# Performance work log

Measured on AMD Instinct MI355X. Metric: run time of the kernel, lower is better.

## Reference

```python
import jax, jax.numpy as jnp
from jax import lax
import numpy as np

B, L = 256, 4096
H, RL, RH = 128, 2, 32   # num_hiddens, residual layers, residual hiddens
K, D = 512, 64           # codebook size, embedding dim
CC = 0.25                # commitment cost


def conv1d(x, w, b=None, stride=1, pad=0, circular=False):
    # x: (N,C,L), w: (O,I,k)
    if circular and pad > 0:
        x = jnp.pad(x, ((0, 0), (0, 0), (pad, pad)), mode='wrap')
        pad = 0
    y = lax.conv_general_dilated(x, w, (stride,), [(pad, pad)],
                                 dimension_numbers=('NCH', 'OIH', 'NCH'))
    return y if b is None else y + b[None, :, None]


def convt1d(x, w, b):
    # PyTorch ConvTranspose1d(k=4, s=2, p=1); w: (I,O,4). out_len = 2*L.
    wt = jnp.flip(jnp.swapaxes(w, 0, 1), -1)  # (O,I,4)
    y = lax.conv_general_dilated(x, wt, (1,), [(2, 2)], lhs_dilation=(2,),
                                 dimension_numbers=('NCH', 'OIH', 'NCH'))
    return y + b[None, :, None]


def res_stack(x, w1s, w2s):
    for i in range(w1s.shape[0]):
        h = conv1d(jax.nn.relu(x), w1s[i], None, 1, 1, circular=True)
        h = conv1d(jax.nn.relu(h), w2s[i], None, 1, 0)
        x = x + h
    return jax.nn.relu(x)


def setup_inputs() -> dict:
    key = jax.random.key(0)
    ks = iter(jax.random.split(key, 64))

    def w(*shape):
        fan_in = int(np.prod(shape[1:]))
        return jax.random.normal(next(ks), shape, jnp.float32) / np.sqrt(fan_in)

    def bias(n):
        return jax.random.uniform(next(ks), (n,), jnp.float32, -0.05, 0.05)

    inp = {'x': jax.random.normal(next(ks), (B, 1, L), jnp.float32)}
    # Encoder
    inp['enc_c1_w'] = w(H // 2, 1, 4);      inp['enc_c1_b'] = bias(H // 2)
    inp['enc_c2_w'] = w(H, H // 2, 4);      inp['enc_c2_b'] = bias(H)
    inp['enc_c3_w'] = w(H, H, 4);           inp['enc_c3_b'] = bias(H)
    inp['enc_c4_w'] = w(H, H, 4);           inp['enc_c4_b'] = bias(H)
    inp['enc_cf_w'] = w(H, H, 3);           inp['enc_cf_b'] = bias(H)
    inp['enc_res_w1'] = w(RL, RH, H, 3)
    inp['enc_res_w2'] = w(RL, H, RH, 1)
    # pre-VQ 1x1 conv
    inp['prevq_w'] = w(D, H, 1);            inp['prevq_b'] = bias(D)
    # codebook: uniform(-1/K, 1/K) as in source
    inp['emb'] = jax.random.uniform(next(ks), (K, D), jnp.float32, -1.0 / K, 1.0 / K)
    # Decoder
    inp['dec_init_w'] = w(H, D, 3);         inp['dec_init_b'] = bias(H)
    inp['dec_res_w1'] = w(RL, RH, H, 3)
    inp['dec_res_w2'] = w(RL, H, RH, 1)
    inp['ct0_w'] = w(H, H, 4);              inp['ct0_b'] = bias(H)
    inp['ct1_w'] = w(H, H, 4);              inp['ct1_b'] = bias(H)
    inp['ct2_w'] = w(H, H // 2, 4);         inp['ct2_b'] = bias(H // 2)
    inp['ct3_w'] = w(H // 2, 1, 4);         inp['ct3_b'] = bias(1)
    return inp


def _forward(x, enc_c1_w, enc_c1_b, enc_c2_w, enc_c2_b, enc_c3_w, enc_c3_b,
             enc_c4_w, enc_c4_b, enc_cf_w, enc_cf_b, enc_res_w1, enc_res_w2,
             prevq_w, prevq_b, emb, dec_init_w, dec_init_b, dec_res_w1,
             dec_res_w2, ct0_w, ct0_b, ct1_w, ct1_b, ct2_w, ct2_b, ct3_w, ct3_b):
    sg = lax.stop_gradient
    relu = jax.nn.relu
    # ---- Encoder (circular padding) ----
    z = relu(conv1d(x, enc_c1_w, enc_c1_b, 2, 1, circular=True))
    z = relu(conv1d(z, enc_c2_w, enc_c2_b, 2, 1, circular=True))
    z = relu(conv1d(z, enc_c3_w, enc_c3_b, 2, 1, circular=True))
    z = relu(conv1d(z, enc_c4_w, enc_c4_b, 2, 1, circular=True))
    z = conv1d(z, enc_cf_w, enc_cf_b, 1, 1, circular=True)
    z = res_stack(z, enc_res_w1, enc_res_w2)
    z = conv1d(z, prevq_w, prevq_b, 1, 0)        # (B, D, T)
    # ---- Vector quantizer ----
    z_t = jnp.transpose(z, (0, 2, 1))            # (B, T, D)
    flat = z_t.reshape(-1, D)                    # (BT, D)
    dist = (jnp.sum(flat ** 2, axis=1, keepdims=True)
            + jnp.sum(emb ** 2, axis=1)
            - 2.0 * flat @ emb.T)                # (BT, K)
    idx = jnp.argmin(dist, axis=1)               # (BT,)
    enc = jax.nn.one_hot(idx, K, dtype=flat.dtype)
    q = (enc @ emb).reshape(z_t.shape)           # (B, T, D)
    e_loss = jnp.mean((sg(q) - z_t) ** 2)
    q_loss = jnp.mean((q - sg(z_t)) ** 2)
    loss = q_loss + CC * e_loss
    q_st = z_t + sg(q - z_t)                     # straight-through
    avg = jnp.mean(enc, axis=0)
    perplexity = jnp.exp(-jnp.sum(avg * jnp.log(avg + 1e-10)))
    quantized = jnp.transpose(q_st, (0, 2, 1))   # (B, D, T)
    # ---- Decoder ----
    h = conv1d(quantized, dec_init_w, dec_init_b, 1, 1)
    h = res_stack(h, dec_res_w1, dec_res_w2)
    h = relu(convt1d(h, ct0_w, ct0_b))
    h = relu(convt1d(h, ct1_w, ct1_b))
    h = relu(convt1d(h, ct2_w, ct2_b))
    x_recon = convt1d(h, ct3_w, ct3_b)           # (B, 1, L)
    return loss, x_recon, perplexity


def reference(x, enc_c1_w, enc_c1_b, enc_c2_w, enc_c2_b, enc_c3_w, enc_c3_b,
              enc_c4_w, enc_c4_b, enc_cf_w, enc_cf_b, enc_res_w1, enc_res_w2,
              prevq_w, prevq_b, emb, dec_init_w, dec_init_b, dec_res_w1,
              dec_res_w2, ct0_w, ct0_b, ct1_w, ct1_b, ct2_w, ct2_b, ct3_w, ct3_b):
    return _forward(x, enc_c1_w, enc_c1_b, enc_c2_w, enc_c2_b, enc_c3_w,
                    enc_c3_b, enc_c4_w, enc_c4_b, enc_cf_w, enc_cf_b,
                    enc_res_w1, enc_res_w2, prevq_w, prevq_b, emb,
                    dec_init_w, dec_init_b, dec_res_w1, dec_res_w2,
                    ct0_w, ct0_b, ct1_w, ct1_b, ct2_w, ct2_b, ct3_w, ct3_b)
```

## Files before the change

### kernel.cpp

```cpp
#include <hip/hip_runtime.h>

#define DEVI __device__ __forceinline__

typedef __bf16 bf16x8 __attribute__((ext_vector_type(8)));
typedef float f32x4 __attribute__((ext_vector_type(4)));

DEVI ushort f2b(float f) {
  uint b = __float_as_uint(f);
  uint r = (b + 0x7FFFu + ((b >> 16) & 1u)) >> 16;
  return (ushort)r;
}
DEVI float b2f(ushort u) { return __uint_as_float(((uint)u) << 16); }

struct PrepArgs {
  int nw;
  int tot[20];
  const float* src[20];
  ushort* dst[20];
  int ci[20], co[20], sco[20], sci[20], sk[20];
};

__global__ __launch_bounds__(256)
void prep_all(PrepArgs a, int total) {
  int i = blockIdx.x * 256 + threadIdx.x;
  if (i >= total) return;
  int w = 0;
  while (i >= a.tot[w]) { i -= a.tot[w]; ++w; }
  const int li = i;
  const int CI = a.ci[w];
  int ciX = i % CI;
  int rest = i / CI;
  int coX = rest % a.co[w];
  int k = rest / a.co[w];
  a.dst[w][li] = f2b(a.src[w][coX * a.sco[w] + ciX * a.sci[w] + k * a.sk[w]]);
}

__global__ __launch_bounds__(256)
void enc1_bf(const float* __restrict__ x, const float* __restrict__ w1,
             const float* __restrict__ b1, ushort* __restrict__ out) {
  __shared__ float xl[516];
  __shared__ float w1s[256];
  __shared__ float b1s[64];
  const int n = blockIdx.x >> 3;
  const int t0 = (blockIdx.x & 7) << 8;
  const int tid = threadIdx.x;
  const float* xb = x + ((size_t)n << 12);
  for (int j = tid; j < 514; j += 256)
    xl[j] = xb[(2 * t0 - 1 + j + 4096) & 4095];
  if (tid < 256) w1s[tid] = w1[tid];
  if (tid < 64) b1s[tid] = b1[tid];
  __syncthreads();

  const int oct = tid & 7;
  float4 w4[8];
  float bs[8];
  #pragma unroll
  for (int e = 0; e < 8; ++e) {
    w4[e] = *reinterpret_cast<const float4*>(&w1s[(oct * 8 + e) * 4]);
    bs[e] = b1s[oct * 8 + e];
  }
  ushort* ob = out + (((size_t)n * 2048 + t0) << 6) + tid * 8;
  #pragma unroll
  for (int it = 0; it < 8; ++it) {
    const int tl = it * 32 + (tid >> 3);
    const float x0 = xl[2 * tl], x1 = xl[2 * tl + 1], x2 = xl[2 * tl + 2], x3 = xl[2 * tl + 3];
    uint pack[4];
    #pragma unroll
    for (int h = 0; h < 4; ++h) {
      float s0 = fmaf(w4[2 * h].x, x0, fmaf(w4[2 * h].y, x1,
                 fmaf(w4[2 * h].z, x2, fmaf(w4[2 * h].w, x3, bs[2 * h]))));
      float s1 = fmaf(w4[2 * h + 1].x, x0, fmaf(w4[2 * h + 1].y, x1,
                 fmaf(w4[2 * h + 1].z, x2, fmaf(w4[2 * h + 1].w, x3, bs[2 * h + 1]))));
      pack[h] = (uint)f2b(fmaxf(s0, 0.0f)) | ((uint)f2b(fmaxf(s1, 0.0f)) << 16);
    }
    *reinterpret_cast<uint4*>(ob + it * 2048) = uint4{pack[0], pack[1], pack[2], pack[3]};
  }
}

template<int CI, int CO, int K, int S, bool CIRC, bool GATHER, int NT, int WAVES_CO,
         int NCHUNK = 1>
__global__ __launch_bounds__(256)
void conv_mfma(const ushort* __restrict__ in, const ushort* __restrict__ wb,
               const float* __restrict__ bias, const ushort* __restrict__ resid,
               ushort* __restrict__ out, const int* __restrict__ gidx,
               int Tin, int in_relu, int out_relu) {
  constexpr int PAD = (K > 1) ? 1 : 0;
  constexpr int TT = NT * 16;
  constexpr int SPAN = S * (TT - 1) + K;
  constexpr int CICH = CI / NCHUNK;
  constexpr int CIGc = CICH / 8;
  constexpr int COT = CO / 16;
  constexpr int WCOT = COT / WAVES_CO;
  constexpr int WAVES_T = 4 / WAVES_CO;
  constexpr int WTT = NT / WAVES_T;
  constexpr int KSH = (S == 2) ? 1 : 0;
  static_assert(CICH % 32 == 0 && COT % WAVES_CO == 0 && NT % WAVES_T == 0, "");

  __shared__ __align__(16) ushort xs[SPAN * CICH];

  const int Tout = Tin / S;
  const int tilesPerB = Tout / TT;
  const int n = blockIdx.x / tilesPerB;
  const int t0 = (blockIdx.x % tilesPerB) * TT;
  const int tid = threadIdx.x;
  const int wid = tid >> 6, lane = tid & 63;
  const int l15 = lane & 15, l4 = lane >> 4;

  const int t_in0 = S * t0 - PAD;
  const ushort* inb = GATHER ? in : in + (size_t)n * Tin * CI;

  const int wco = wid % WAVES_CO;
  const int wt = wid / WAVES_CO;
  const int co_base = wco * WCOT * 16;
  const int t_base = wt * WTT * 16;

  f32x4 acc[WTT][WCOT] = {};

  for (int h = 0; h < NCHUNK; ++h) {
    if (h) __syncthreads();
    for (int i = tid; i < SPAN * CIGc; i += 256) {
      int t = i / CIGc, g = i - (i / CIGc) * CIGc;
      int tg = t_in0 + t;
      uint4 v;
      if (CIRC) {
        tg = (tg < 0) ? tg + Tin : (tg >= Tin ? tg - Tin : tg);
        v = *reinterpret_cast<const uint4*>(inb + (size_t)tg * CI + h * CICH + g * 8);
      } else if (GATHER) {
        if ((unsigned)tg < (unsigned)Tin) {
          int id = gidx[n * Tin + tg];
          v = *reinterpret_cast<const uint4*>(inb + (size_t)id * CI + h * CICH + g * 8);
        } else
          v = uint4{0, 0, 0, 0};
      } else {
        if ((unsigned)tg < (unsigned)Tin)
          v = *reinterpret_cast<const uint4*>(inb + (size_t)tg * CI + h * CICH + g * 8);
        else
          v = uint4{0, 0, 0, 0};
      }
      if (in_relu) {
        ushort* pv = reinterpret_cast<ushort*>(&v);
        #pragma unroll
        for (int e = 0; e < 8; ++e) pv[e] = (pv[e] & 0x8000) ? 0 : pv[e];
      }
      *reinterpret_cast<uint4*>(&xs[t * CICH + ((g ^ ((t >> KSH) & (CIGc - 1))) * 8)]) = v;
    }
    __syncthreads();

    for (int cc = 0; cc < CICH / 32; ++cc) {
      const int ccg = h * (CICH / 32) + cc;
      bf16x8 bk[K][WCOT];
      #pragma unroll
      for (int k = 0; k < K; ++k)
        #pragma unroll
        for (int c = 0; c < WCOT; ++c)
          bk[k][c] = __builtin_bit_cast(bf16x8, *reinterpret_cast<const uint4*>(
              wb + (size_t)((k * CO + co_base + c * 16 + l15)) * CI + ccg * 32 + l4 * 8));
      #pragma unroll
      for (int k = 0; k < K; ++k) {
        #pragma unroll
        for (int tt2 = 0; tt2 < WTT; ++tt2) {
          int trow = S * (t_base + tt2 * 16 + l15) + k;
          int g = cc * 4 + l4;
          bf16x8 afr = __builtin_bit_cast(bf16x8, *reinterpret_cast<const uint4*>(
              &xs[trow * CICH + ((g ^ ((trow >> KSH) & (CIGc - 1))) * 8)]));
          #pragma unroll
          for (int c = 0; c < WCOT; ++c)
            acc[tt2][c] = __builtin_amdgcn_mfma_f32_16x16x32_bf16(afr, bk[k][c], acc[tt2][c], 0, 0, 0);
        }
      }
    }
  }

  float bv[WCOT];
  #pragma unroll
  for (int c = 0; c < WCOT; ++c)
    bv[c] = bias ? bias[co_base + c * 16 + l15] : 0.0f;
  ushort* outb = out + (size_t)n * Tout * CO;
  const ushort* resb = resid ? resid + (size_t)n * Tout * CO : nullptr;
  #pragma unroll
  for (int tt2 = 0; tt2 < WTT; ++tt2)
    #pragma unroll
    for (int c = 0; c < WCOT; ++c)
      #pragma unroll
      for (int r = 0; r < 4; ++r) {
        int t = t0 + t_base + tt2 * 16 + 4 * l4 + r;
        int co = co_base + c * 16 + l15;
        float v = acc[tt2][c][r] + bv[c];
        if (resb) v += b2f(resb[(size_t)t * CO + co]);
        if (out_relu) v = fmaxf(v, 0.0f);
        outb[(size_t)t * CO + co] = f2b(v);
      }
}

__global__ __launch_bounds__(256)
void res_mfma(const ushort* __restrict__ in, const ushort* __restrict__ wb1,
              const ushort* __restrict__ wb2, ushort* __restrict__ out) {
  constexpr int CI = 128, CIG = 16;
  constexpr int TT = 64, SPAN = 66, Tin = 256;
  __shared__ __align__(16) ushort xs[SPAN * CI];
  ushort* hs = xs;
  const int n = blockIdx.x >> 2;
  const int t0 = (blockIdx.x & 3) * TT;
  const int tid = threadIdx.x;
  const int wid = tid >> 6, lane = tid & 63;
  const int l15 = lane & 15, l4 = lane >> 4;
  const int t_in0 = t0 - 1;
  const ushort* inb = in + (size_t)n * Tin * CI;

  for (int i = tid; i < SPAN * CIG; i += 256) {
    int t = i >> 4, g = i & 15;
    int tg = t_in0 + t;
    tg = (tg < 0) ? tg + Tin : (tg >= Tin ? tg - Tin : tg);
    uint4 v = *reinterpret_cast<const uint4*>(inb + (size_t)tg * CI + g * 8);
    ushort* pv = reinterpret_cast<ushort*>(&v);
    #pragma unroll
    for (int e = 0; e < 8; ++e) pv[e] = (pv[e] & 0x8000) ? 0 : pv[e];
    *reinterpret_cast<uint4*>(&xs[t * CI + ((g ^ (t & 15)) * 8)]) = v;
  }
  __syncthreads();

  f32x4 acc1[2] = {};
  for (int cc = 0; cc < 4; ++cc)
    #pragma unroll
    for (int k = 0; k < 3; ++k) {
      bf16x8 bfr[2];
      #pragma unroll
      for (int c = 0; c < 2; ++c)
        bfr[c] = __builtin_bit_cast(bf16x8, *reinterpret_cast<const uint4*>(
            wb1 + (size_t)((k * 32 + c * 16 + l15)) * CI + cc * 32 + l4 * 8));
      int trow = wid * 16 + l15 + k;
      int g = cc * 4 + l4;
      bf16x8 afr = __builtin_bit_cast(bf16x8, *reinterpret_cast<const uint4*>(
          &xs[trow * CI + ((g ^ (trow & 15)) * 8)]));
      acc1[0] = __builtin_amdgcn_mfma_f32_16x16x32_bf16(afr, bfr[0], acc1[0], 0, 0, 0);
      acc1[1] = __builtin_amdgcn_mfma_f32_16x16x32_bf16(afr, bfr[1], acc1[1], 0, 0, 0);
    }
  __syncthreads();
  #pragma unroll
  for (int c = 0; c < 2; ++c)
    #pragma unroll
    for (int r = 0; r < 4; ++r) {
      float v = acc1[c][r];
      hs[(wid * 16 + l4 * 4 + r) * 40 + c * 16 + l15] = (v > 0.0f) ? f2b(v) : (ushort)0;
    }
  __syncthreads();

  {
    bf16x8 afr = *reinterpret_cast<const bf16x8*>(&hs[(wid * 16 + l15) * 40 + l4 * 8]);
    f32x4 acc[8];
    #pragma unroll
    for (int c = 0; c < 8; ++c) {
      bf16x8 bfr = __builtin_bit_cast(bf16x8, *reinterpret_cast<const uint4*>(
          wb2 + (size_t)(c * 16 + l15) * 32 + l4 * 8));
      f32x4 z = {};
      acc[c] = __builtin_amdgcn_mfma_f32_16x16x32_bf16(afr, bfr, z, 0, 0, 0);
    }
    ushort* outb = out + (size_t)n * Tin * CI;
    #pragma unroll
    for (int c = 0; c < 8; ++c)
      #pragma unroll
      for (int r = 0; r < 4; ++r) {
        int t = t0 + wid * 16 + l4 * 4 + r;
        int co = c * 16 + l15;
        float v = acc[c][r] + b2f(inb[(size_t)t * CI + co]);
        outb[(size_t)t * CI + co] = f2b(v);
      }
  }
}

template<int CO>
__global__ __launch_bounds__(256)
void convt_mfma(const ushort* __restrict__ in, const ushort* __restrict__ wb,
                const float* __restrict__ bias, ushort* __restrict__ out,
                int Tin, int in_relu, int out_relu) {
  constexpr int CI = 128, CIG = 16;
  constexpr int NT = 4, TT = 64;
  constexpr int SPAN = TT + 2;
  constexpr int COT = CO / 16;
  constexpr int WCOT = (COT + 3) / 4;
  constexpr int WAVES_CO = COT / WCOT;
  constexpr int WTT = NT;

  __shared__ __align__(16) ushort xs[SPAN * CI];

  const int Tout = 2 * Tin;
  const int tilesPerB = Tin / TT;
  const int n = blockIdx.x / tilesPerB;
  const int tp0 = (blockIdx.x % tilesPerB) * TT;
  const int tid = threadIdx.x;
  const int wid = tid >> 6, lane = tid & 63;
  const int l15 = lane & 15, l4 = lane >> 4;

  const int t_in0 = tp0 - 1;
  const ushort* inb = in + (size_t)n * Tin * CI;
  for (int i = tid; i < SPAN * CIG; i += 256) {
    int t = i >> 4, g = i & 15;
    int tg = t_in0 + t;
    uint4 v;
    if ((unsigned)tg < (unsigned)Tin)
      v = *reinterpret_cast<const uint4*>(inb + (size_t)tg * CI + g * 8);
    else
      v = uint4{0, 0, 0, 0};
    if (in_relu) {
      ushort* pv = reinterpret_cast<ushort*>(&v);
      #pragma unroll
      for (int e = 0; e < 8; ++e) pv[e] = (pv[e] & 0x8000) ? 0 : pv[e];
    }
    *reinterpret_cast<uint4*>(&xs[t * CI + ((g ^ (t & 15)) * 8)]) = v;
  }
  __syncthreads();

  const int wco = wid % WAVES_CO;
  const int co_base = wco * WCOT * 16;

  f32x4 accE[WTT][WCOT] = {};
  f32x4 accO[WTT][WCOT] = {};

  for (int cc = 0; cc < 4; ++cc) {
    bf16x8 bk[4][WCOT];
    #pragma unroll
    for (int k = 0; k < 4; ++k)
      #pragma unroll
      for (int c = 0; c < WCOT; ++c)
        bk[k][c] = __builtin_bit_cast(bf16x8, *reinterpret_cast<const uint4*>(
            wb + (size_t)((k * CO + co_base + c * 16 + l15)) * CI + cc * 32 + l4 * 8));
    #pragma unroll
    for (int tt2 = 0; tt2 < WTT; ++tt2) {
      int lt = tt2 * 16 + l15 + 1;
      int g = cc * 4 + l4;
      bf16x8 a0 = __builtin_bit_cast(bf16x8, *reinterpret_cast<const uint4*>(
          &xs[lt * CI + ((g ^ (lt & 15)) * 8)]));
      bf16x8 am = __builtin_bit_cast(bf16x8, *reinterpret_cast<const uint4*>(
          &xs[(lt - 1) * CI + ((g ^ ((lt - 1) & 15)) * 8)]));
      bf16x8 ap = __builtin_bit_cast(bf16x8, *reinterpret_cast<const uint4*>(
          &xs[(lt + 1) * CI + ((g ^ ((lt + 1) & 15)) * 8)]));
      #pragma unroll
      for (int c = 0; c < WCOT; ++c) {
        accE[tt2][c] = __builtin_amdgcn_mfma_f32_16x16x32_bf16(a0, bk[1][c], accE[tt2][c], 0, 0, 0);
        accE[tt2][c] = __builtin_amdgcn_mfma_f32_16x16x32_bf16(am, bk[3][c], accE[tt2][c], 0, 0, 0);
        accO[tt2][c] = __builtin_amdgcn_mfma_f32_16x16x32_bf16(ap, bk[0][c], accO[tt2][c], 0, 0, 0);
        accO[tt2][c] = __builtin_amdgcn_mfma_f32_16x16x32_bf16(a0, bk[2][c], accO[tt2][c], 0, 0, 0);
      }
    }
  }

  float bv[WCOT];
  #pragma unroll
  for (int c = 0; c < WCOT; ++c) bv[c] = bias[co_base + c * 16 + l15];
  ushort* outb = out + (size_t)n * Tout * CO;
  #pragma unroll
  for (int tt2 = 0; tt2 < WTT; ++tt2)
    #pragma unroll
    for (int c = 0; c < WCOT; ++c)
      #pragma unroll
      for (int r = 0; r < 4; ++r) {
        int tp = tp0 + tt2 * 16 + 4 * l4 + r;
        int co = co_base + c * 16 + l15;
        float vE = accE[tt2][c][r] + bv[c];
        float vO = accO[tt2][c][r] + bv[c];
        if (out_relu) { vE = fmaxf(vE, 0.0f); vO = fmaxf(vO, 0.0f); }
        outb[(size_t)(2 * tp) * CO + co] = f2b(vE);
        outb[(size_t)(2 * tp + 1) * CO + co] = f2b(vO);
      }
}

__global__ __launch_bounds__(256)
void ct23_mfma(const ushort* __restrict__ in, const ushort* __restrict__ wb,
               const float* __restrict__ bias, const float* __restrict__ w3,
               const float* __restrict__ b3, float* __restrict__ out) {
  constexpr int CI = 128, CO = 64, CIG = 16;
  constexpr int TT = 64, SPAN = 66, Tin = 1024;
  __shared__ __align__(16) ushort buf[8580];
  __shared__ float2 w3p[2][64];
  ushort* xs = buf;
  ushort* ys = buf;

  const int n = blockIdx.x >> 4;
  const int tp0 = (blockIdx.x & 15) * TT;
  const int tid = threadIdx.x;
  const int wid = tid >> 6, lane = tid & 63;
  const int l15 = lane & 15, l4 = lane >> 4;
  const int t_in0 = tp0 - 1;
  const ushort* inb = in + (size_t)n * Tin * CI;

  if (tid < 128) {
    int parity = tid >> 6, ci = tid & 63;
    w3p[parity][ci] = parity
        ? float2{w3[ci * 4 + 0], w3[ci * 4 + 2]}
        : float2{w3[ci * 4 + 1], w3[ci * 4 + 3]};
  }
  for (int i = tid; i < SPAN * CIG; i += 256) {
    int t = i >> 4, g = i & 15;
    int tg = t_in0 + t;
    uint4 v;
    if ((unsigned)tg < (unsigned)Tin)
      v = *reinterpret_cast<const uint4*>(inb + (size_t)tg * CI + g * 8);
    else
      v = uint4{0, 0, 0, 0};
    *reinterpret_cast<uint4*>(&xs[t * CI + ((g ^ (t & 15)) * 8)]) = v;
  }
  __syncthreads();

  const int co = wid * 16 + l15;
  f32x4 accE[4] = {}, accO[4] = {};
  f32x4 hO = {}, hE = {};

  for (int cc = 0; cc < 4; ++cc) {
    bf16x8 bk[4];
    #pragma unroll
    for (int k = 0; k < 4; ++k)
      bk[k] = __builtin_bit_cast(bf16x8, *reinterpret_cast<const uint4*>(
          wb + (size_t)((k * CO + co)) * CI + cc * 32 + l4 * 8));
    const int g = cc * 4 + l4;
    auto rd = [&](int lt) -> bf16x8 {
      return __builtin_bit_cast(bf16x8, *reinterpret_cast<const uint4*>(
          &xs[lt * CI + ((g ^ (lt & 15)) * 8)]));
    };
    #pragma unroll
    for (int tt2 = 0; tt2 < 4; ++tt2) {
      int lt = tt2 * 16 + l15 + 1;
      bf16x8 a0 = rd(lt), am = rd(lt - 1), ap = rd(lt + 1);
      accE[tt2] = __builtin_amdgcn_mfma_f32_16x16x32_bf16(a0, bk[1], accE[tt2], 0, 0, 0);
      accE[tt2] = __builtin_amdgcn_mfma_f32_16x16x32_bf16(am, bk[3], accE[tt2], 0, 0, 0);
      accO[tt2] = __builtin_amdgcn_mfma_f32_16x16x32_bf16(ap, bk[0], accO[tt2], 0, 0, 0);
      accO[tt2] = __builtin_amdgcn_mfma_f32_16x16x32_bf16(a0, bk[2], accO[tt2], 0, 0, 0);
    }
    bf16x8 h0 = rd(0), h1 = rd(1), h64 = rd(64), h65 = rd(65);
    hO = __builtin_amdgcn_mfma_f32_16x16x32_bf16(h1, bk[0], hO, 0, 0, 0);
    hO = __builtin_amdgcn_mfma_f32_16x16x32_bf16(h0, bk[2], hO, 0, 0, 0);
    hE = __builtin_amdgcn_mfma_f32_16x16x32_bf16(h65, bk[1], hE, 0, 0, 0);
    hE = __builtin_amdgcn_mfma_f32_16x16x32_bf16(h64, bk[3], hE, 0, 0, 0);
  }
  __syncthreads();

  const float bv = bias[co];
  #pragma unroll
  for (int tt2 = 0; tt2 < 4; ++tt2)
    #pragma unroll
    for (int r = 0; r < 4; ++r) {
      int m = tt2 * 16 + 4 * l4 + r;
      ys[(2 * m + 1) * 66 + co] = f2b(fmaxf(accE[tt2][r] + bv, 0.0f));
      ys[(2 * m + 2) * 66 + co] = f2b(fmaxf(accO[tt2][r] + bv, 0.0f));
    }
  if (l4 == 0) {
    ys[co]            = (tp0 == 0) ? (ushort)0 : f2b(fmaxf(hO[0] + bv, 0.0f));
    ys[129 * 66 + co] = (tp0 + TT == Tin) ? (ushort)0 : f2b(fmaxf(hE[0] + bv, 0.0f));
  }
  __syncthreads();

  const int o = 4 * tp0 + tid;
  const int odd = tid & 1;
  const int ha = (tid + odd) >> 1;
  const ushort* ra = &ys[(ha + 1) * 66];
  const ushort* rb = &ys[ha * 66];
  const float2* wp = w3p[odd];
  float s = b3[0];
  #pragma unroll
  for (int c = 0; c < 32; ++c) {
    uint va = *reinterpret_cast<const uint*>(ra + 2 * c);
    uint vb = *reinterpret_cast<const uint*>(rb + 2 * c);
    float2 w0 = wp[2 * c], w1 = wp[2 * c + 1];
    s = fmaf(w0.x, __uint_as_float(va << 16), s);
    s = fmaf(w1.x, __uint_as_float(va & 0xFFFF0000u), s);
    s = fmaf(w0.y, __uint_as_float(vb << 16), s);
    s = fmaf(w1.y, __uint_as_float(vb & 0xFFFF0000u), s);
  }
  out[(size_t)n * 4096 + o] = s;
}

__global__ __launch_bounds__(256)
void vq_mfma(const ushort* __restrict__ zt, const ushort* __restrict__ embb,
             int* __restrict__ idx, int* __restrict__ hist,
             float* __restrict__ loss_accum) {
  __shared__ __align__(16) ushort es[512 * 64];
  __shared__ float eel[512];
  __shared__ int lhist[512];
  const int tid = threadIdx.x;
  const int wid = tid >> 6, lane = tid & 63;
  const int l15 = lane & 15, l4 = lane >> 4;

  for (int i = tid; i < 512 * 8; i += 256) {
    int c = i >> 3, g = i & 7;
    uint4 v = reinterpret_cast<const uint4*>(embb)[i];
    reinterpret_cast<uint4*>(es)[c * 8 + (g ^ (c & 7))] = v;
    const ushort* pv = reinterpret_cast<const ushort*>(&v);
    float ss = 0.0f;
    #pragma unroll
    for (int e = 0; e < 8; ++e) { float f = b2f(pv[e]); ss = fmaf(f, f, ss); }
    ss += __shfl_xor(ss, 1);
    ss += __shfl_xor(ss, 2);
    ss += __shfl_xor(ss, 4);
    if ((i & 7) == 0) eel[c] = ss;
  }
  for (int i = tid; i < 512; i += 256) lhist[i] = 0;
  __syncthreads();

  const int rb = blockIdx.x * 256 + wid * 64;
  bf16x8 bz[4][2];
  float zz[4], best[4];
  int bi[4];
  #pragma unroll
  for (int rt = 0; rt < 4; ++rt) {
    const int r = rb + rt * 16 + l15;
    uint4 v0 = *reinterpret_cast<const uint4*>(zt + (size_t)r * 64 + l4 * 8);
    uint4 v1 = *reinterpret_cast<const uint4*>(zt + (size_t)r * 64 + 32 + l4 * 8);
    bz[rt][0] = __builtin_bit_cast(bf16x8, v0);
    bz[rt][1] = __builtin_bit_cast(bf16x8, v1);
    float s = 0.0f;
    const ushort* p0 = reinterpret_cast<const ushort*>(&v0);
    const ushort* p1 = reinterpret_cast<const ushort*>(&v1);
    #pragma unroll
    for (int e = 0; e < 8; ++e) {
      float f0 = b2f(p0[e]), f1 = b2f(p1[e]);
      s = fmaf(f0, f0, fmaf(f1, f1, s));
    }
    s += __shfl_xor(s, 16);
    s += __shfl_xor(s, 32);
    zz[rt] = s;
    best[rt] = 3.4e38f;
    bi[rt] = 0;
  }

  for (int ct = 0; ct < 32; ++ct) {
    const int c = ct * 16 + l15;
    bf16x8 a0 = __builtin_bit_cast(bf16x8, reinterpret_cast<const uint4*>(es)[
        c * 8 + (l4 ^ (c & 7))]);
    bf16x8 a1 = __builtin_bit_cast(bf16x8, reinterpret_cast<const uint4*>(es)[
        c * 8 + ((4 | l4) ^ (c & 7))]);
    #pragma unroll
    for (int rt = 0; rt < 4; ++rt) {
      f32x4 acc = {};
      acc = __builtin_amdgcn_mfma_f32_16x16x32_bf16(a0, bz[rt][0], acc, 0, 0, 0);
      acc = __builtin_amdgcn_mfma_f32_16x16x32_bf16(a1, bz[rt][1], acc, 0, 0, 0);
      #pragma unroll
      for (int rr = 0; rr < 4; ++rr) {
        int code = ct * 16 + l4 * 4 + rr;
        float d = eel[code] - 2.0f * acc[rr];
        if (d < best[rt] || (d == best[rt] && code < bi[rt])) { best[rt] = d; bi[rt] = code; }
      }
    }
  }
  float vsum = 0.0f;
  #pragma unroll
  for (int rt = 0; rt < 4; ++rt) {
    #pragma unroll
    for (int m = 16; m <= 32; m <<= 1) {
      float ob = __shfl_xor(best[rt], m);
      int oi = __shfl_xor(bi[rt], m);
      if (ob < best[rt] || (ob == best[rt] && oi < bi[rt])) { best[rt] = ob; bi[rt] = oi; }
    }
    if (l4 == 0) {
      idx[rb + rt * 16 + l15] = bi[rt];
      atomicAdd(&lhist[bi[rt]], 1);
      vsum += zz[rt] + best[rt];
    }
  }
  #pragma unroll
  for (int m = 1; m < 64; m <<= 1) vsum += __shfl_xor(vsum, m);
  if (lane == 0) atomicAdd(loss_accum, vsum);
  __syncthreads();
  for (int i = tid; i < 512; i += 256)
    if (lhist[i]) atomicAdd(&hist[i], lhist[i]);
}

__global__ __launch_bounds__(512)
void finalize(const int* __restrict__ hist, const float* __restrict__ loss_accum,
              float* __restrict__ out) {
  __shared__ float red[8];
  int tid = threadIdx.x;
  float avg = (float)hist[tid] * (1.0f / 65536.0f);
  float v = avg * logf(avg + 1e-10f);
  for (int off = 32; off > 0; off >>= 1) v += __shfl_down(v, off);
  if ((tid & 63) == 0) red[tid >> 6] = v;
  __syncthreads();
  if (tid == 0) {
    float s = 0.0f;
    for (int i = 0; i < 8; ++i) s += red[i];
    out[1048577] = expf(-s);
    out[0] = 1.25f * loss_accum[0] * (1.0f / (65536.0f * 64.0f));
  }
}

extern "C" void kernel_launch(void* const* d_in, const int* in_sizes, int n_in,
                              void* d_out, int out_size, void* d_ws, size_t ws_size,
                              hipStream_t stream) {
  (void)in_sizes; (void)n_in; (void)out_size; (void)ws_size;
  const float* x    = (const float*)d_in[0];
  const float* c1w  = (const float*)d_in[1];
  const float* c1b  = (const float*)d_in[2];
  const float* c2w  = (const float*)d_in[3];
  const float* c2b  = (const float*)d_in[4];
  const float* c3w  = (const float*)d_in[5];
  const float* c3b  = (const float*)d_in[6];
  const float* c4w  = (const float*)d_in[7];
  const float* c4b  = (const float*)d_in[8];
  const float* cfw  = (const float*)d_in[9];
  const float* cfb  = (const float*)d_in[10];
  const float* erw1 = (const float*)d_in[11];
  const float* erw2 = (const float*)d_in[12];
  const float* pqw  = (const float*)d_in[13];
  const float* pqb  = (const float*)d_in[14];
  const float* emb  = (const float*)d_in[15];
  const float* diw  = (const float*)d_in[16];
  const float* dib  = (const float*)d_in[17];
  const float* drw1 = (const float*)d_in[18];
  const float* drw2 = (const float*)d_in[19];
  const float* t0w  = (const float*)d_in[20];
  const float* t0b  = (const float*)d_in[21];
  const float* t1w  = (const float*)d_in[22];
  const float* t1b  = (const float*)d_in[23];
  const float* t2w  = (const float*)d_in[24];
  const float* t2b  = (const float*)d_in[25];
  const float* t3w  = (const float*)d_in[26];
  const float* t3b  = (const float*)d_in[27];

  char* wsb = (char*)d_ws;
  ushort* R0 = (ushort*)wsb;
  ushort* R1 = (ushort*)(wsb + 67108864);
  ushort* R2 = (ushort*)(wsb + 134217728);
  ushort* R3 = (ushort*)(wsb + 0);
  ushort* R4 = (ushort*)(wsb + 16777216);
  ushort* R6 = (ushort*)(wsb + 37748736);
  ushort* WPu = (ushort*)(wsb + 167772160);
  ushort* wb_e2 = WPu + 0;
  ushort* wb_e3 = WPu + 32768;
  ushort* wb_e4 = WPu + 98304;
  ushort* wb_cf = WPu + 163840;
  ushort* wb_r1a = WPu + 212992;
  ushort* wb_r1b = WPu + 225280;
  ushort* wb_r2a = WPu + 237568;
  ushort* wb_r2b = WPu + 241664;
  ushort* wb_pq = WPu + 245760;
  ushort* wb_di = WPu + 253952;
  ushort* wb_d1a = WPu + 278528;
  ushort* wb_d1b = WPu + 290816;
  ushort* wb_d2a = WPu + 303104;
  ushort* wb_d2b = WPu + 307200;
  ushort* wb_t0 = WPu + 311296;
  ushort* wb_t1 = WPu + 376832;
  ushort* wb_t2 = WPu + 442368;
  ushort* wb_emb = WPu + 475136;
  char* fp = wsb + 167772160 + 1048576;
  int*   idxb  = (int*)(fp + 2048);
  int*   histb = (int*)(fp + 2048 + 262144);
  float* lossb = (float*)(fp + 2048 + 262144 + 2048);
  float* outp  = (float*)d_out;

  hipMemsetAsync(histb, 0, 512 * sizeof(int), stream);
  hipMemsetAsync(lossb, 0, sizeof(float), stream);

  PrepArgs pa{};
  int nw = 0, total = 0;
  auto addw = [&](const float* src, ushort* dst, int CO, int CI, int K,
                  int sco, int sci, int sk) {
    pa.tot[nw] = K * CO * CI; pa.src[nw] = src; pa.dst[nw] = dst;
    pa.ci[nw] = CI; pa.co[nw] = CO; pa.sco[nw] = sco; pa.sci[nw] = sci; pa.sk[nw] = sk;
    total += pa.tot[nw]; ++nw;
  };
  addw(c2w, wb_e2, 128, 64, 4, 256, 4, 1);
  addw(c3w, wb_e3, 128, 128, 4, 512, 4, 1);
  addw(c4w, wb_e4, 128, 128, 4, 512, 4, 1);
  addw(cfw, wb_cf, 128, 128, 3, 384, 3, 1);
  addw(erw1, wb_r1a, 32, 128, 3, 384, 3, 1);
  addw(erw1 + 12288, wb_r1b, 32, 128, 3, 384, 3, 1);
  addw(erw2, wb_r2a, 128, 32, 1, 32, 1, 1);
  addw(erw2 + 4096, wb_r2b, 128, 32, 1, 32, 1, 1);
  addw(pqw, wb_pq, 64, 128, 1, 128, 1, 1);
  addw(diw, wb_di, 128, 64, 3, 192, 3, 1);
  addw(drw1, wb_d1a, 32, 128, 3, 384, 3, 1);
  addw(drw1 + 12288, wb_d1b, 32, 128, 3, 384, 3, 1);
  addw(drw2, wb_d2a, 128, 32, 1, 32, 1, 1);
  addw(drw2 + 4096, wb_d2b, 128, 32, 1, 32, 1, 1);
  addw(t0w, wb_t0, 128, 128, 4, 4, 512, 1);
  addw(t1w, wb_t1, 128, 128, 4, 4, 512, 1);
  addw(t2w, wb_t2, 64, 128, 4, 4, 256, 1);
  addw(emb, wb_emb, 512, 64, 1, 64, 1, 1);
  pa.nw = nw;
  prep_all<<<(total + 255) / 256, 256, 0, stream>>>(pa, total);

  enc1_bf<<<2048, 256, 0, stream>>>(x, c1w, c1b, R0);
  conv_mfma<64, 128, 4, 2, true, false, 4, 4><<<4096, 256, 0, stream>>>(R0, wb_e2, c2b, nullptr, R1, nullptr, 2048, 0, 1);
  conv_mfma<128, 128, 4, 2, true, false, 4, 4, 2><<<2048, 256, 0, stream>>>(R1, wb_e3, c3b, nullptr, R2, nullptr, 1024, 0, 1);
  conv_mfma<128, 128, 4, 2, true, false, 4, 4, 2><<<1024, 256, 0, stream>>>(R2, wb_e4, c4b, nullptr, R3, nullptr, 512, 0, 1);
  conv_mfma<128, 128, 3, 1, true, false, 8, 2><<<512, 256, 0, stream>>>(R3, wb_cf, cfb, nullptr, R4, nullptr, 256, 0, 0);
  res_mfma<<<1024, 256, 0, stream>>>(R4, wb_r1a, wb_r2a, R3);
  res_mfma<<<1024, 256, 0, stream>>>(R3, wb_r1b, wb_r2b, R4);
  conv_mfma<128, 64, 1, 1, false, false, 8, 2><<<512, 256, 0, stream>>>(R4, wb_pq, pqb, nullptr, R6, nullptr, 256, 1, 0);
  vq_mfma<<<256, 256, 0, stream>>>(R6, wb_emb, idxb, histb, lossb);
  finalize<<<1, 512, 0, stream>>>(histb, lossb, outp);
  conv_mfma<64, 128, 3, 1, false, true, 8, 2><<<512, 256, 0, stream>>>(wb_emb, wb_di, dib, nullptr, R3, idxb, 256, 0, 0);
  res_mfma<<<1024, 256, 0, stream>>>(R3, wb_d1a, wb_d2a, R4);
  res_mfma<<<1024, 256, 0, stream>>>(R4, wb_d1b, wb_d2b, R3);
  convt_mfma<128><<<1024, 256, 0, stream>>>(R3, wb_t0, t0b, R2, 256, 1, 1);
  convt_mfma<128><<<2048, 256, 0, stream>>>(R2, wb_t1, t1b, R0, 512, 0, 1);
  ct23_mfma<<<4096, 256, 0, stream>>>(R0, wb_t2, t2b, t3w, t3b, outp + 1);
}
```

Measured before the change: 442.5 us.

## Fuse first two encoder convolutions into one MFMA kernel via shared-memory intermediate

Merges the scalar first conv (1->64 channels) and the second strided conv (64->128) into a single kernel. The conv1 output tile, including halo, is computed into XOR-swizzled LDS and consumed directly by bf16 MFMA for conv2. This removes the write and re-read of the large 64-channel bf16 intermediate in global memory and one kernel launch. In exchange, each block recomputes a small halo of conv1 outputs, and the output stores are scalar per-element rather than vectorized.

```diff
diff --git a/kernel.cpp b/kernel.cpp
--- a/kernel.cpp
+++ b/kernel.cpp
@@ -36,45 +36,99 @@
 }
 
 __global__ __launch_bounds__(256)
-void enc1_bf(const float* __restrict__ x, const float* __restrict__ w1,
-             const float* __restrict__ b1, ushort* __restrict__ out) {
-  __shared__ float xl[516];
+void enc12_mfma(const float* __restrict__ x, const float* __restrict__ w1,
+                const float* __restrict__ b1, const ushort* __restrict__ wb,
+                const float* __restrict__ b2, ushort* __restrict__ out) {
+  constexpr int CI = 64, CO = 128, K = 4, TT = 64;
+  constexpr int SPAN = 2 * (TT - 1) + K;
+  __shared__ __align__(16) ushort xs[SPAN * CI];
+  __shared__ float xl[264];
   __shared__ float w1s[256];
   __shared__ float b1s[64];
-  const int n = blockIdx.x >> 3;
-  const int t0 = (blockIdx.x & 7) << 8;
+
+  const int n = blockIdx.x >> 4;
+  const int t0 = (blockIdx.x & 15) * TT;
   const int tid = threadIdx.x;
+  const int wid = tid >> 6, lane = tid & 63;
+  const int l15 = lane & 15, l4 = lane >> 4;
+
+  const int t_in0 = 2 * t0 - 1;
+  const int xw0 = 2 * t_in0 - 1;
   const float* xb = x + ((size_t)n << 12);
-  for (int j = tid; j < 514; j += 256)
-    xl[j] = xb[(2 * t0 - 1 + j + 4096) & 4095];
+
+  for (int j = tid; j < 262; j += 256)
+    xl[j] = xb[(xw0 + j + 8192) & 4095];
   if (tid < 256) w1s[tid] = w1[tid];
   if (tid < 64) b1s[tid] = b1[tid];
   __syncthreads();
 
-  const int oct = tid & 7;
-  float4 w4[8];
+  const int g = tid & 7;
+  float4 wv[8];
   float bs[8];
   #pragma unroll
   for (int e = 0; e < 8; ++e) {
-    w4[e] = *reinterpret_cast<const float4*>(&w1s[(oct * 8 + e) * 4]);
-    bs[e] = b1s[oct * 8 + e];
-  }
-  ushort* ob = out + (((size_t)n * 2048 + t0) << 6) + tid * 8;
-  #pragma unroll
-  for (int it = 0; it < 8; ++it) {
-    const int tl = it * 32 + (tid >> 3);
-    const float x0 = xl[2 * tl], x1 = xl[2 * tl + 1], x2 = xl[2 * tl + 2], x3 = xl[2 * tl + 3];
-    uint pack[4];
-    #pragma unroll
-    for (int h = 0; h < 4; ++h) {
-      float s0 = fmaf(w4[2 * h].x, x0, fmaf(w4[2 * h].y, x1,
-                 fmaf(w4[2 * h].z, x2, fmaf(w4[2 * h].w, x3, bs[2 * h]))));
-      float s1 = fmaf(w4[2 * h + 1].x, x0, fmaf(w4[2 * h + 1].y, x1,
-                 fmaf(w4[2 * h + 1].z, x2, fmaf(w4[2 * h + 1].w, x3, bs[2 * h + 1]))));
-      pack[h] = (uint)f2b(fmaxf(s0, 0.0f)) | ((uint)f2b(fmaxf(s1, 0.0f)) << 16);
-    }
-    *reinterpret_cast<uint4*>(ob + it * 2048) = uint4{pack[0], pack[1], pack[2], pack[3]};
-  }
+    wv[e] = *reinterpret_cast<const float4*>(&w1s[(g * 8 + e) * 4]);
+    bs[e] = b1s[g * 8 + e];
+  }
+  #pragma unroll
+  for (int it = 0; it < 5; ++it) {
+    int t = it * 32 + (tid >> 3);
+    if (t < SPAN) {
+      float x0 = xl[2 * t], x1 = xl[2 * t + 1], x2 = xl[2 * t + 2], x3 = xl[2 * t + 3];
+      uint pack[4];
+      #pragma unroll
+      for (int h = 0; h < 4; ++h) {
+        float s0 = fmaf(wv[2 * h].x, x0, fmaf(wv[2 * h].y, x1,
+                   fmaf(wv[2 * h].z, x2, fmaf(wv[2 * h].w, x3, bs[2 * h]))));
+        float s1 = fmaf(wv[2 * h + 1].x, x0, fmaf(wv[2 * h + 1].y, x1,
+                   fmaf(wv[2 * h + 1].z, x2, fmaf(wv[2 * h + 1].w, x3, bs[2 * h + 1]))));
+        pack[h] = (uint)f2b(fmaxf(s0, 0.0f)) | ((uint)f2b(fmaxf(s1, 0.0f)) << 16);
+      }
+      *reinterpret_cast<uint4*>(&xs[t * CI + ((g ^ ((t >> 1) & 7)) * 8)]) =
+          uint4{pack[0], pack[1], pack[2], pack[3]};
+    }
+  }
+  __syncthreads();
+
+  const int wco = wid;
+  const int co_base = wco * 32;
+  f32x4 acc[4][2] = {};
+  for (int cc = 0; cc < 2; ++cc) {
+    bf16x8 bk[K][2];
+    #pragma unroll
+    for (int k = 0; k < K; ++k)
+      #pragma unroll
+      for (int c = 0; c < 2; ++c)
+        bk[k][c] = __builtin_bit_cast(bf16x8, *reinterpret_cast<const uint4*>(
+            wb + (size_t)((k * CO + co_base + c * 16 + l15)) * CI + cc * 32 + l4 * 8));
+    #pragma unroll
+    for (int k = 0; k < K; ++k) {
+      #pragma unroll
+      for (int tt2 = 0; tt2 < 4; ++tt2) {
+        int trow = 2 * (tt2 * 16 + l15) + k;
+        int gg = cc * 4 + l4;
+        bf16x8 afr = __builtin_bit_cast(bf16x8, *reinterpret_cast<const uint4*>(
+            &xs[trow * CI + ((gg ^ ((trow >> 1) & 7)) * 8)]));
+        #pragma unroll
+        for (int c = 0; c < 2; ++c)
+          acc[tt2][c] = __builtin_amdgcn_mfma_f32_16x16x32_bf16(afr, bk[k][c], acc[tt2][c], 0, 0, 0);
+      }
+    }
+  }
+  float bv[2];
+  #pragma unroll
+  for (int c = 0; c < 2; ++c) bv[c] = b2[co_base + c * 16 + l15];
+  ushort* outb = out + (size_t)n * 1024 * CO;
+  #pragma unroll
+  for (int tt2 = 0; tt2 < 4; ++tt2)
+    #pragma unroll
+    for (int c = 0; c < 2; ++c)
+      #pragma unroll
+      for (int r = 0; r < 4; ++r) {
+        int t = t0 + tt2 * 16 + 4 * l4 + r;
+        int co = co_base + c * 16 + l15;
+        outb[(size_t)t * CO + co] = f2b(fmaxf(acc[tt2][c][r] + bv[c], 0.0f));
+      }
 }
 
 template<int CI, int CO, int K, int S, bool CIRC, bool GATHER, int NT, int WAVES_CO,
@@ -678,8 +732,7 @@
   pa.nw = nw;
   prep_all<<<(total + 255) / 256, 256, 0, stream>>>(pa, total);
 
-  enc1_bf<<<2048, 256, 0, stream>>>(x, c1w, c1b, R0);
-  conv_mfma<64, 128, 4, 2, true, false, 4, 4><<<4096, 256, 0, stream>>>(R0, wb_e2, c2b, nullptr, R1, nullptr, 2048, 0, 1);
+  enc12_mfma<<<4096, 256, 0, stream>>>(x, c1w, c1b, wb_e2, c2b, R1);
   conv_mfma<128, 128, 4, 2, true, false, 4, 4, 2><<<2048, 256, 0, stream>>>(R1, wb_e3, c3b, nullptr, R2, nullptr, 1024, 0, 1);
   conv_mfma<128, 128, 4, 2, true, false, 4, 4, 2><<<1024, 256, 0, stream>>>(R2, wb_e4, c4b, nullptr, R3, nullptr, 512, 0, 1);
   conv_mfma<128, 128, 3, 1, true, false, 8, 2><<<512, 256, 0, stream>>>(R3, wb_cf, cfb, nullptr, R4, nullptr, 256, 0, 0);
```

New measurement: 417.4 us. 5.7% less time.
